# Kernel tuning notes

Measured on AMD Instinct MI355X. Metric: run time of the kernel, lower is better.

Reference implementation:

```python
import jax, jax.numpy as jnp
import numpy as np

# Layered NEAT genome: inputs, 4 hidden layers, outputs. Every non-input node
# has FAN_IN incoming connections from the previous layer; weights are the
# per-connection scalar parameters of the original nn.ParameterDict.
LAYER_SIZES = [256, 512, 512, 512, 512, 64]
FAN_IN = 32
BATCH = 2048
OFFSETS = np.cumsum([0] + LAYER_SIZES)  # node-id offsets per layer


def _build_edges(seed=0):
    """Edge list (src node id, dst node id) in topological (layer) order."""
    rng = np.random.default_rng(seed)
    src, dst = [], []
    for l in range(1, len(LAYER_SIZES)):
        s = rng.integers(OFFSETS[l - 1], OFFSETS[l], size=(LAYER_SIZES[l], FAN_IN))
        d = np.repeat(np.arange(OFFSETS[l], OFFSETS[l + 1]), FAN_IN)
        src.append(s.ravel())
        dst.append(d)
    return (np.concatenate(src).astype(np.int32),
            np.concatenate(dst).astype(np.int32))


def setup_inputs() -> dict:
    key = jax.random.key(0)
    k1, k2 = jax.random.split(key)
    src, dst = _build_edges()
    x = jax.random.normal(k1, (BATCH, LAYER_SIZES[0]), dtype=jnp.float32)
    w = jax.random.normal(k2, (src.shape[0],), dtype=jnp.float32) * 0.5
    return {"x": x, "w": w, "src": jnp.asarray(src), "dst": jnp.asarray(dst)}


def reference(x, w, src, dst):
    n_nodes = int(OFFSETS[-1])
    B = x.shape[0]
    # node_outputs dict -> dense [B, n_nodes] activation buffer
    acts = jnp.zeros((B, n_nodes), dtype=x.dtype).at[:, :LAYER_SIZES[0]].set(x)
    e0 = 0
    for l in range(1, len(LAYER_SIZES)):  # fixed small layer count
        E = LAYER_SIZES[l] * FAN_IN
        s = src[e0:e0 + E]
        d = dst[e0:e0 + E] - OFFSETS[l]          # local node index within layer
        msgs = acts[:, s] * w[e0:e0 + E]          # [B, E] per-connection products
        sums = jnp.zeros((B, LAYER_SIZES[l]), dtype=x.dtype).at[:, d].add(msgs)
        acts = acts.at[:, OFFSETS[l]:OFFSETS[l + 1]].set(jax.nn.sigmoid(sums))
        e0 += E
    # stack output node activations, [B, n_outputs]
    return acts[:, OFFSETS[-2]:OFFSETS[-1]]
```

## Files before the change

### kernel.cpp

```cpp
#include <hip/hip_runtime.h>
#include <hip/hip_fp16.h>


typedef _Float16 half8_t  __attribute__((ext_vector_type(8)));
typedef float    float8_t __attribute__((ext_vector_type(8)));

constexpr int TB    = 8;
constexpr int BLOCK = 512;
constexpr int E_TOT = 67584;

__global__ void pack_edges(const int* __restrict__ src, const float* __restrict__ w,
                           unsigned* __restrict__ rec)
{
    const int o = blockIdx.x * 256 + threadIdx.x;
    if (o >= E_TOT) return;
    int e0, offPrev;
    if      (o < 16384) { e0 = 0;     offPrev = 0;    }
    else if (o < 32768) { e0 = 16384; offPrev = 256;  }
    else if (o < 49152) { e0 = 32768; offPrev = 768;  }
    else if (o < 65536) { e0 = 49152; offPrev = 1280; }
    else                { e0 = 65536; offPrev = 1792; }
    const int ol = o - e0;
    int eid;
    if (e0 == 65536) {
        const int q = ol & 3, r = ol >> 2;
        const int c = r >> 6, n = r & 63;
        eid = e0 + n * 32 + c * 4 + q;
    } else {
        const int q = ol & 3, t = ol >> 2;
        const int i = t & 63, c = (t >> 6) & 7, g = t >> 9;
        eid = e0 + (g * 64 + i) * 32 + c * 4 + q;
    }
    const unsigned off = (unsigned)(src[eid] - offPrev) * (TB * 2);
    const unsigned hw  = (unsigned)__half_as_ushort(__float2half(w[eid]));
    rec[o] = off | (hw << 16);
}

__device__ __forceinline__ float sigmoidf(float s)
{
    return __fdividef(1.0f, 1.0f + __expf(-s));
}

template<bool PACKED>
__global__ __launch_bounds__(BLOCK) void neat_fwd(
    const float* __restrict__ x,
    const float* __restrict__ w,
    const int*   __restrict__ src,
    const int4*  __restrict__ rp,
    float*       __restrict__ out)
{
    __shared__ __align__(16) _Float16 bufA[512 * TB];
    __shared__ __align__(16) _Float16 bufB[512 * TB];
    __shared__ float l5p[512 * 9];

    const int tid    = threadIdx.x;
    const int batch0 = blockIdx.x * TB;

    {
        const int r  = tid >> 6;
        const int c4 = (tid & 63) * 4;
        const float4 v = *(const float4*)(x + (size_t)(batch0 + r) * 256 + c4);
        bufA[(c4 + 0) * TB + r] = (_Float16)v.x;
        bufA[(c4 + 1) * TB + r] = (_Float16)v.y;
        bufA[(c4 + 2) * TB + r] = (_Float16)v.z;
        bufA[(c4 + 3) * TB + r] = (_Float16)v.w;
    }
    __syncthreads();

    _Float16* prev = bufA;
    _Float16* cur  = bufB;

    const int base = (tid >> 6) * 512 + (tid & 63);

#define EDGE(RR, ACC)                                                          \
    do {                                                                       \
        const unsigned rr = (unsigned)(RR);                                    \
        const float wf = __half2float(__ushort_as_half((unsigned short)(rr >> 16))); \
        const half8_t a = *(const half8_t*)(pv + (rr & 0xffffu));              \
        _Pragma("unroll")                                                      \
        for (int k = 0; k < 8; ++k)                                            \
            ACC[k] = fmaf((float)a[k], wf, ACC[k]);                            \
    } while (0)

#define EDGE_RAW(SRCID, WF, ACC)                                               \
    do {                                                                       \
        const float wf = (WF);                                                 \
        const half8_t a = *(const half8_t*)(pv + (unsigned)((SRCID) - offPrev) * (TB * 2)); \
        _Pragma("unroll")                                                      \
        for (int k = 0; k < 8; ++k)                                            \
            ACC[k] = fmaf((float)a[k], wf, ACC[k]);                            \
    } while (0)

#pragma unroll
    for (int l = 0; l < 4; ++l) {
        const char* pv = (const char*)prev;
        float8_t acc = {0.f, 0.f, 0.f, 0.f, 0.f, 0.f, 0.f, 0.f};
        if (PACKED) {
            const int4* rl = rp + l * 4096;
#pragma unroll
            for (int c = 0; c < 8; ++c) {
                const int4 r4 = rl[base + c * 64];
                EDGE(r4.x, acc);
                EDGE(r4.y, acc);
                EDGE(r4.z, acc);
                EDGE(r4.w, acc);
            }
        } else {
            const int e0 = l * 16384;
            const int offPrev = (l == 0) ? 0 : (256 + (l - 1) * 512);
            const int ebase = e0 + tid * 32;
#pragma unroll
            for (int c = 0; c < 8; ++c) {
                const int4   s4 = *(const int4*)(src + ebase + c * 4);
                const float4 w4 = *(const float4*)(w + ebase + c * 4);
                EDGE_RAW(s4.x, w4.x, acc);
                EDGE_RAW(s4.y, w4.y, acc);
                EDGE_RAW(s4.z, w4.z, acc);
                EDGE_RAW(s4.w, w4.w, acc);
            }
        }
        half8_t r;
#pragma unroll
        for (int k = 0; k < 8; ++k)
            r[k] = (_Float16)sigmoidf(acc[k]);
        *(half8_t*)(cur + tid * TB) = r;
        __syncthreads();
        _Float16* t = prev; prev = cur; cur = t;
    }

    {
        const char* pv = (const char*)prev;
        float8_t acc = {0.f, 0.f, 0.f, 0.f, 0.f, 0.f, 0.f, 0.f};
        if (PACKED) {
            const int4 r4 = rp[16384 + tid];
            EDGE(r4.x, acc);
            EDGE(r4.y, acc);
            EDGE(r4.z, acc);
            EDGE(r4.w, acc);
        } else {
            const int n = tid & 63, c = tid >> 6;
            const int offPrev = 1792;
            const int eb = 65536 + n * 32 + c * 4;
            const int4   s4 = *(const int4*)(src + eb);
            const float4 w4 = *(const float4*)(w + eb);
            EDGE_RAW(s4.x, w4.x, acc);
            EDGE_RAW(s4.y, w4.y, acc);
            EDGE_RAW(s4.z, w4.z, acc);
            EDGE_RAW(s4.w, w4.w, acc);
        }
        float* dst = l5p + tid * 9;
#pragma unroll
        for (int k = 0; k < 8; ++k)
            dst[k] = acc[k];
    }
    __syncthreads();

    {
        const int n = tid & 63;
        const int b = tid >> 6;
        float s = 0.f;
#pragma unroll
        for (int c = 0; c < 8; ++c)
            s += l5p[(c * 64 + n) * 9 + b];
        out[(size_t)(batch0 + b) * 64 + n] = sigmoidf(s);
    }
#undef EDGE
#undef EDGE_RAW
}

extern "C" void kernel_launch(void* const* d_in, const int* in_sizes, int n_in,
                              void* d_out, int out_size, void* d_ws, size_t ws_size,
                              hipStream_t stream)
{
    const float* x   = (const float*)d_in[0];
    const float* w   = (const float*)d_in[1];
    const int*   src = (const int*)d_in[2];
    float* out = (float*)d_out;

    const int batch = in_sizes[0] / 256;
    const int grid  = batch / TB;

    unsigned* rec = (unsigned*)d_ws;

    if (ws_size >= (size_t)E_TOT * 4) {
        pack_edges<<<(E_TOT + 255) / 256, 256, 0, stream>>>(src, w, rec);
        neat_fwd<true><<<grid, BLOCK, 0, stream>>>(x, w, src, (const int4*)rec, out);
    } else {
        neat_fwd<false><<<grid, BLOCK, 0, stream>>>(x, w, src, (const int4*)rec, out);
    }
}
```

Baseline: 21.31 us.

## Split each hidden node's fan-in across two threads with 1024-thread blocks

Doubles the block to 1024 threads so each hidden node's 32 incoming edges are split between two threads of 16 edges each. Partial sums from the upper half go through shared memory and are combined before the sigmoid. The edge packing is reordered to match the new per-half access pattern. The goal is more latency-hiding parallelism per CU, at the cost of an extra barrier per layer, idle upper-half threads in the output stages, and 1024-thread blocks that may limit occupancy and register budget.

After: 23.47 us. 10.2% more time.

```diff
diff --git a/kernel.cpp b/kernel.cpp
--- a/kernel.cpp
+++ b/kernel.cpp
@@ -6,7 +6,7 @@
 typedef float    float8_t __attribute__((ext_vector_type(8)));
 
 constexpr int TB    = 8;
-constexpr int BLOCK = 512;
+constexpr int BLOCK = 1024;
 constexpr int E_TOT = 67584;
 
 __global__ void pack_edges(const int* __restrict__ src, const float* __restrict__ w,
@@ -14,22 +14,27 @@
 {
     const int o = blockIdx.x * 256 + threadIdx.x;
     if (o >= E_TOT) return;
-    int e0, offPrev;
-    if      (o < 16384) { e0 = 0;     offPrev = 0;    }
-    else if (o < 32768) { e0 = 16384; offPrev = 256;  }
-    else if (o < 49152) { e0 = 32768; offPrev = 768;  }
-    else if (o < 65536) { e0 = 49152; offPrev = 1280; }
-    else                { e0 = 65536; offPrev = 1792; }
-    const int ol = o - e0;
-    int eid;
-    if (e0 == 65536) {
+    int eid, offPrev;
+    if (o < 65536) {
+        const int layer = o >> 14;
+        const int e0    = layer << 14;
+        offPrev = (layer == 0) ? 0 : (256 + (layer - 1) * 512);
+        const int ol = o - e0;
+        const int q  = ol & 3;
+        const int t  = ol >> 2;
+        const int i  = t & 63;
+        const int t2 = t >> 6;
+        const int h  = t2 & 1;
+        const int t3 = t2 >> 1;
+        const int c  = t3 & 3;
+        const int g  = t3 >> 2;
+        eid = e0 + (g * 64 + i) * 32 + h * 16 + c * 4 + q;
+    } else {
+        offPrev = 1792;
+        const int ol = o - 65536;
         const int q = ol & 3, r = ol >> 2;
         const int c = r >> 6, n = r & 63;
-        eid = e0 + n * 32 + c * 4 + q;
-    } else {
-        const int q = ol & 3, t = ol >> 2;
-        const int i = t & 63, c = (t >> 6) & 7, g = t >> 9;
-        eid = e0 + (g * 64 + i) * 32 + c * 4 + q;
+        eid = 65536 + n * 32 + c * 4 + q;
     }
     const unsigned off = (unsigned)(src[eid] - offPrev) * (TB * 2);
     const unsigned hw  = (unsigned)__half_as_ushort(__float2half(w[eid]));
@@ -42,7 +47,7 @@
 }
 
 template<bool PACKED>
-__global__ __launch_bounds__(BLOCK) void neat_fwd(
+__global__ __launch_bounds__(BLOCK, 1) void neat_fwd(
     const float* __restrict__ x,
     const float* __restrict__ w,
     const int*   __restrict__ src,
@@ -51,12 +56,14 @@
 {
     __shared__ __align__(16) _Float16 bufA[512 * TB];
     __shared__ __align__(16) _Float16 bufB[512 * TB];
-    __shared__ float l5p[512 * 9];
+    __shared__ __align__(16) float scratch[512 * 12];
 
     const int tid    = threadIdx.x;
+    const int n      = tid & 511;
+    const int h      = tid >> 9;
     const int batch0 = blockIdx.x * TB;
 
-    {
+    if (tid < 512) {
         const int r  = tid >> 6;
         const int c4 = (tid & 63) * 4;
         const float4 v = *(const float4*)(x + (size_t)(batch0 + r) * 256 + c4);
@@ -70,7 +77,8 @@
     _Float16* prev = bufA;
     _Float16* cur  = bufB;
 
-    const int base = (tid >> 6) * 512 + (tid & 63);
+    const int g = n >> 6, i = n & 63;
+    const int base = g * 512 + h * 64 + i;
 
 #define EDGE(RR, ACC)                                                          \
     do {                                                                       \
@@ -98,8 +106,8 @@
         if (PACKED) {
             const int4* rl = rp + l * 4096;
 #pragma unroll
-            for (int c = 0; c < 8; ++c) {
-                const int4 r4 = rl[base + c * 64];
+            for (int c = 0; c < 4; ++c) {
+                const int4 r4 = rl[base + c * 128];
                 EDGE(r4.x, acc);
                 EDGE(r4.y, acc);
                 EDGE(r4.z, acc);
@@ -108,9 +116,9 @@
         } else {
             const int e0 = l * 16384;
             const int offPrev = (l == 0) ? 0 : (256 + (l - 1) * 512);
-            const int ebase = e0 + tid * 32;
-#pragma unroll
-            for (int c = 0; c < 8; ++c) {
+            const int ebase = e0 + n * 32 + h * 16;
+#pragma unroll
+            for (int c = 0; c < 4; ++c) {
                 const int4   s4 = *(const int4*)(src + ebase + c * 4);
                 const float4 w4 = *(const float4*)(w + ebase + c * 4);
                 EDGE_RAW(s4.x, w4.x, acc);
@@ -119,16 +127,32 @@
                 EDGE_RAW(s4.w, w4.w, acc);
             }
         }
-        half8_t r;
-#pragma unroll
-        for (int k = 0; k < 8; ++k)
-            r[k] = (_Float16)sigmoidf(acc[k]);
-        *(half8_t*)(cur + tid * TB) = r;
+        if (h == 1) {
+            float* d = scratch + n * 12;
+            *(float4*)(d + 0) = make_float4(acc[0], acc[1], acc[2], acc[3]);
+            *(float4*)(d + 4) = make_float4(acc[4], acc[5], acc[6], acc[7]);
+        }
+        __syncthreads();
+        if (h == 0) {
+            const float* s = scratch + n * 12;
+            const float4 p0 = *(const float4*)(s + 0);
+            const float4 p1 = *(const float4*)(s + 4);
+            half8_t r;
+            r[0] = (_Float16)sigmoidf(acc[0] + p0.x);
+            r[1] = (_Float16)sigmoidf(acc[1] + p0.y);
+            r[2] = (_Float16)sigmoidf(acc[2] + p0.z);
+            r[3] = (_Float16)sigmoidf(acc[3] + p0.w);
+            r[4] = (_Float16)sigmoidf(acc[4] + p1.x);
+            r[5] = (_Float16)sigmoidf(acc[5] + p1.y);
+            r[6] = (_Float16)sigmoidf(acc[6] + p1.z);
+            r[7] = (_Float16)sigmoidf(acc[7] + p1.w);
+            *(half8_t*)(cur + n * TB) = r;
+        }
         __syncthreads();
         _Float16* t = prev; prev = cur; cur = t;
     }
 
-    {
+    if (tid < 512) {
         const char* pv = (const char*)prev;
         float8_t acc = {0.f, 0.f, 0.f, 0.f, 0.f, 0.f, 0.f, 0.f};
         if (PACKED) {
@@ -138,9 +162,9 @@
             EDGE(r4.z, acc);
             EDGE(r4.w, acc);
         } else {
-            const int n = tid & 63, c = tid >> 6;
+            const int nn = tid & 63, c = tid >> 6;
             const int offPrev = 1792;
-            const int eb = 65536 + n * 32 + c * 4;
+            const int eb = 65536 + nn * 32 + c * 4;
             const int4   s4 = *(const int4*)(src + eb);
             const float4 w4 = *(const float4*)(w + eb);
             EDGE_RAW(s4.x, w4.x, acc);
@@ -148,21 +172,20 @@
             EDGE_RAW(s4.z, w4.z, acc);
             EDGE_RAW(s4.w, w4.w, acc);
         }
-        float* dst = l5p + tid * 9;
-#pragma unroll
-        for (int k = 0; k < 8; ++k)
-            dst[k] = acc[k];
+        float* d = scratch + tid * 12;
+        *(float4*)(d + 0) = make_float4(acc[0], acc[1], acc[2], acc[3]);
+        *(float4*)(d + 4) = make_float4(acc[4], acc[5], acc[6], acc[7]);
     }
     __syncthreads();
 
-    {
-        const int n = tid & 63;
-        const int b = tid >> 6;
+    if (tid < 512) {
+        const int nn = tid & 63;
+        const int b  = tid >> 6;
         float s = 0.f;
 #pragma unroll
         for (int c = 0; c < 8; ++c)
-            s += l5p[(c * 64 + n) * 9 + b];
-        out[(size_t)(batch0 + b) * 64 + n] = sigmoidf(s);
+            s += scratch[(c * 64 + nn) * 12 + b];
+        out[(size_t)(batch0 + b) * 64 + nn] = sigmoidf(s);
     }
 #undef EDGE
 #undef EDGE_RAW
```

## Reorder per-node edge schedule to spread LDS gathers across banks

Applied to the files above, without the earlier changes.

Replaces the plain edge packing kernel with a scheduler that reorders each node's 32 incoming edges by source bank class. Within each step, lanes of a wavefront then read from distinct LDS bank groups, which is meant to cut bank conflicts in the half8 gathers of the main kernel. Edges that overflow their bank slot are placed in the leftover slots. The packing kernel becomes more complex, using shared atomics and popcount logic.

Result: no change. 21.14 us (-0.8%).

```diff
diff --git a/kernel.cpp b/kernel.cpp
--- a/kernel.cpp
+++ b/kernel.cpp
@@ -9,31 +9,95 @@
 constexpr int BLOCK = 512;
 constexpr int E_TOT = 67584;
 
-__global__ void pack_edges(const int* __restrict__ src, const float* __restrict__ w,
-                           unsigned* __restrict__ rec)
-{
-    const int o = blockIdx.x * 256 + threadIdx.x;
-    if (o >= E_TOT) return;
-    int e0, offPrev;
-    if      (o < 16384) { e0 = 0;     offPrev = 0;    }
-    else if (o < 32768) { e0 = 16384; offPrev = 256;  }
-    else if (o < 49152) { e0 = 32768; offPrev = 768;  }
-    else if (o < 65536) { e0 = 49152; offPrev = 1280; }
-    else                { e0 = 65536; offPrev = 1792; }
-    const int ol = o - e0;
-    int eid;
-    if (e0 == 65536) {
-        const int q = ol & 3, r = ol >> 2;
-        const int c = r >> 6, n = r & 63;
-        eid = e0 + n * 32 + c * 4 + q;
-    } else {
-        const int q = ol & 3, t = ol >> 2;
-        const int i = t & 63, c = (t >> 6) & 7, g = t >> 9;
-        eid = e0 + (g * 64 + i) * 32 + c * 4 + q;
-    }
-    const unsigned off = (unsigned)(src[eid] - offPrev) * (TB * 2);
-    const unsigned hw  = (unsigned)__half_as_ushort(__float2half(w[eid]));
-    rec[o] = off | (hw << 16);
+__device__ __forceinline__ unsigned nth_set_bit(unsigned m, int o)
+{
+    unsigned p = 0, r = (unsigned)o + 1, c;
+    c = __popc(m & 0xFFFFu); if (r > c) { r -= c; m >>= 16; p += 16; }
+    c = __popc(m & 0xFFu);   if (r > c) { r -= c; m >>= 8;  p += 8;  }
+    c = __popc(m & 0xFu);    if (r > c) { r -= c; m >>= 4;  p += 4;  }
+    c = __popc(m & 0x3u);    if (r > c) { r -= c; m >>= 2;  p += 2;  }
+    c = __popc(m & 0x1u);    if (r > c) { p += 1; }
+    return p;
+}
+
+__device__ __forceinline__ unsigned rep_bits(int k)
+{
+    unsigned v = 0;
+    v = (k > 0) ? 0x00000001u : v;
+    v = (k > 1) ? 0x00000101u : v;
+    v = (k > 2) ? 0x00010101u : v;
+    v = (k > 3) ? 0x01010101u : v;
+    return v;
+}
+
+__global__ __launch_bounds__(256) void pack_sched(const int* __restrict__ src,
+                                                  const float* __restrict__ w,
+                                                  unsigned* __restrict__ rec)
+{
+    __shared__ unsigned pl[8][4];
+
+    const int t  = blockIdx.x * 256 + threadIdx.x;
+    const int j  = t & 31;
+    const int nb = threadIdx.x >> 5;
+
+    int L, n, offPrev, lane;
+    if (t < 65536) {
+        L = t >> 14;
+        offPrev = (L == 0) ? 0 : (256 + (L - 1) * 512);
+        n = (t >> 5) & 511;
+        lane = n & 63;
+    } else {
+        L = 4; offPrev = 1792;
+        n = (t - 65536) >> 5;
+        lane = n;
+    }
+
+    if (threadIdx.x < 32)
+        ((unsigned*)pl)[threadIdx.x] = 0;
+    __syncthreads();
+
+    const int      s    = src[t] - offPrev;
+    const unsigned c    = (unsigned)s & 7u;
+    const unsigned vrec = ((unsigned)(s << 4)) |
+                          ((unsigned)__half_as_ushort(__float2half(w[t])) << 16);
+
+    atomicOr(&pl[nb][0], (c & 1u) << j);
+    atomicOr(&pl[nb][1], ((c >> 1) & 1u) << j);
+    atomicOr(&pl[nb][2], ((c >> 2) & 1u) << j);
+    __syncthreads();
+
+    const unsigned p0 = pl[nb][0], p1 = pl[nb][1], p2 = pl[nb][2];
+
+    unsigned taken = 0;
+    int ovfBefore = 0;
+#pragma unroll
+    for (int cc = 0; cc < 8; ++cc) {
+        const unsigned m = ((cc & 1) ? p0 : ~p0) & ((cc & 2) ? p1 : ~p1) & ((cc & 4) ? p2 : ~p2);
+        const int cnt = __popc(m);
+        const int k   = cnt < 4 ? cnt : 4;
+        taken |= rep_bits(k) << ((cc - lane) & 7);
+        ovfBefore += ((unsigned)cc < c) ? (cnt > 4 ? cnt - 4 : 0) : 0;
+    }
+
+    const unsigned mc = ((c & 1) ? p0 : ~p0) & ((c & 2) ? p1 : ~p1) & ((c & 4) ? p2 : ~p2);
+    const int q = __popc(mc & ((1u << j) - 1u));
+
+    int t2;
+    if (q < 4) {
+        t2 = q * 8 + (int)((c - (unsigned)lane) & 7u);
+    } else {
+        t2 = (int)nth_set_bit(~taken, ovfBefore + (q - 4));
+    }
+
+    int pos;
+    if (L < 4) {
+        const int g = n >> 6, i = n & 63, cch = t2 >> 2, qq = t2 & 3;
+        pos = (L << 14) + (((g * 8 + cch) * 64 + i) << 2) + qq;
+    } else {
+        const int cch = t2 >> 2, qq = t2 & 3;
+        pos = 65536 + ((cch * 64 + n) << 2) + qq;
+    }
+    rec[pos] = vrec;
 }
 
 __device__ __forceinline__ float sigmoidf(float s)
@@ -183,7 +247,7 @@
     unsigned* rec = (unsigned*)d_ws;
 
     if (ws_size >= (size_t)E_TOT * 4) {
-        pack_edges<<<(E_TOT + 255) / 256, 256, 0, stream>>>(src, w, rec);
+        pack_sched<<<E_TOT / 256, 256, 0, stream>>>(src, w, rec);
         neat_fwd<true><<<grid, BLOCK, 0, stream>>>(x, w, src, (const int4*)rec, out);
     } else {
         neat_fwd<false><<<grid, BLOCK, 0, stream>>>(x, w, src, (const int4*)rec, out);
```

## Prefetch next layer's edge records into registers and shuffle-reduce final layer

Applied to the files above, without the earlier changes.

Loads of packed edge records for the next layer are issued before the current layer's compute, so global-load latency overlaps the LDS gather and FMA work. The output layer's edge packing is reordered so that 8 consecutive lanes own one output node. Its partial sums are then reduced with wavefront xor-shuffles instead of an LDS staging buffer plus an extra barrier. The cost is roughly 32 more live VGPRs for the rnxt buffer, which could reduce occupancy or cause spills.

Result: no change. 20.96 us, median of 2 (-1.7%).

```diff
diff --git a/kernel.cpp b/kernel.cpp
--- a/kernel.cpp
+++ b/kernel.cpp
@@ -9,29 +9,26 @@
 constexpr int BLOCK = 512;
 constexpr int E_TOT = 67584;
 
-__global__ void pack_edges(const int* __restrict__ src, const float* __restrict__ w,
-                           unsigned* __restrict__ rec)
+__global__ __launch_bounds__(256) void pack_edges(const int* __restrict__ src,
+                                                  const float* __restrict__ w,
+                                                  unsigned* __restrict__ rec)
 {
     const int o = blockIdx.x * 256 + threadIdx.x;
     if (o >= E_TOT) return;
-    int e0, offPrev;
-    if      (o < 16384) { e0 = 0;     offPrev = 0;    }
-    else if (o < 32768) { e0 = 16384; offPrev = 256;  }
-    else if (o < 49152) { e0 = 32768; offPrev = 768;  }
-    else if (o < 65536) { e0 = 49152; offPrev = 1280; }
-    else                { e0 = 65536; offPrev = 1792; }
-    const int ol = o - e0;
-    int eid;
-    if (e0 == 65536) {
-        const int q = ol & 3, r = ol >> 2;
-        const int c = r >> 6, n = r & 63;
-        eid = e0 + n * 32 + c * 4 + q;
-    } else {
+    int eid, offPrev;
+    if (o < 65536) {
+        const int layer = o >> 14;
+        const int e0    = layer << 14;
+        offPrev = (layer == 0) ? 0 : (256 + (layer - 1) * 512);
+        const int ol = o - e0;
         const int q = ol & 3, t = ol >> 2;
         const int i = t & 63, c = (t >> 6) & 7, g = t >> 9;
         eid = e0 + (g * 64 + i) * 32 + c * 4 + q;
-    }
-    const unsigned off = (unsigned)(src[eid] - offPrev) * (TB * 2);
+    } else {
+        offPrev = 1792;
+        eid = o;
+    }
+    const unsigned off = (unsigned)(src[eid] - offPrev) * 16u;
     const unsigned hw  = (unsigned)__half_as_ushort(__float2half(w[eid]));
     rec[o] = off | (hw << 16);
 }
@@ -51,10 +48,16 @@
 {
     __shared__ __align__(16) _Float16 bufA[512 * TB];
     __shared__ __align__(16) _Float16 bufB[512 * TB];
-    __shared__ float l5p[512 * 9];
 
     const int tid    = threadIdx.x;
     const int batch0 = blockIdx.x * TB;
+    const int base   = (tid >> 6) * 512 + (tid & 63);
+
+    int4 rcur[8], rnxt[8];
+    if (PACKED) {
+#pragma unroll
+        for (int c = 0; c < 8; ++c) rcur[c] = rp[base + c * 64];
+    }
 
     {
         const int r  = tid >> 6;
@@ -69,8 +72,6 @@
 
     _Float16* prev = bufA;
     _Float16* cur  = bufB;
-
-    const int base = (tid >> 6) * 512 + (tid & 63);
 
 #define EDGE(RR, ACC)                                                          \
     do {                                                                       \
@@ -85,7 +86,7 @@
 #define EDGE_RAW(SRCID, WF, ACC)                                               \
     do {                                                                       \
         const float wf = (WF);                                                 \
-        const half8_t a = *(const half8_t*)(pv + (unsigned)((SRCID) - offPrev) * (TB * 2)); \
+        const half8_t a = *(const half8_t*)(pv + (unsigned)((SRCID) - offPrev) * 16u); \
         _Pragma("unroll")                                                      \
         for (int k = 0; k < 8; ++k)                                            \
             ACC[k] = fmaf((float)a[k], wf, ACC[k]);                            \
@@ -93,13 +94,22 @@
 
 #pragma unroll
     for (int l = 0; l < 4; ++l) {
+        if (PACKED) {
+            if (l < 3) {
+                const int4* rn = rp + (l + 1) * 4096;
+#pragma unroll
+                for (int c = 0; c < 8; ++c) rnxt[c] = rn[base + c * 64];
+            } else {
+                rnxt[0] = rp[16384 + tid];
+            }
+        }
+
         const char* pv = (const char*)prev;
         float8_t acc = {0.f, 0.f, 0.f, 0.f, 0.f, 0.f, 0.f, 0.f};
         if (PACKED) {
-            const int4* rl = rp + l * 4096;
 #pragma unroll
             for (int c = 0; c < 8; ++c) {
-                const int4 r4 = rl[base + c * 64];
+                const int4 r4 = rcur[c];
                 EDGE(r4.x, acc);
                 EDGE(r4.y, acc);
                 EDGE(r4.z, acc);
@@ -119,6 +129,7 @@
                 EDGE_RAW(s4.w, w4.w, acc);
             }
         }
+
         half8_t r;
 #pragma unroll
         for (int k = 0; k < 8; ++k)
@@ -126,21 +137,25 @@
         *(half8_t*)(cur + tid * TB) = r;
         __syncthreads();
         _Float16* t = prev; prev = cur; cur = t;
+
+        if (PACKED) {
+#pragma unroll
+            for (int c = 0; c < 8; ++c) rcur[c] = rnxt[c];
+        }
     }
 
     {
         const char* pv = (const char*)prev;
         float8_t acc = {0.f, 0.f, 0.f, 0.f, 0.f, 0.f, 0.f, 0.f};
         if (PACKED) {
-            const int4 r4 = rp[16384 + tid];
+            const int4 r4 = rcur[0];
             EDGE(r4.x, acc);
             EDGE(r4.y, acc);
             EDGE(r4.z, acc);
             EDGE(r4.w, acc);
         } else {
-            const int n = tid & 63, c = tid >> 6;
             const int offPrev = 1792;
-            const int eb = 65536 + n * 32 + c * 4;
+            const int eb = 65536 + tid * 4;
             const int4   s4 = *(const int4*)(src + eb);
             const float4 w4 = *(const float4*)(w + eb);
             EDGE_RAW(s4.x, w4.x, acc);
@@ -148,21 +163,18 @@
             EDGE_RAW(s4.z, w4.z, acc);
             EDGE_RAW(s4.w, w4.w, acc);
         }
-        float* dst = l5p + tid * 9;
-#pragma unroll
-        for (int k = 0; k < 8; ++k)
-            dst[k] = acc[k];
-    }
-    __syncthreads();
-
-    {
-        const int n = tid & 63;
-        const int b = tid >> 6;
-        float s = 0.f;
-#pragma unroll
-        for (int c = 0; c < 8; ++c)
-            s += l5p[(c * 64 + n) * 9 + b];
-        out[(size_t)(batch0 + b) * 64 + n] = sigmoidf(s);
+#pragma unroll
+        for (int m = 1; m <= 4; m <<= 1) {
+#pragma unroll
+            for (int k = 0; k < 8; ++k)
+                acc[k] += __shfl_xor(acc[k], m, 64);
+        }
+        if ((tid & 7) == 0) {
+            const int n = tid >> 3;
+#pragma unroll
+            for (int b = 0; b < 8; ++b)
+                out[(size_t)(batch0 + b) * 64 + n] = sigmoidf(acc[b]);
+        }
     }
 #undef EDGE
 #undef EDGE_RAW
```
